# Kernel tuning notes

Hardware: AMD Instinct MI355X
Metric: run time of the kernel (lower is better)

The kernel has to match this reference:

```python
import jax, jax.numpy as jnp
import numpy as np

N_NODES = 50000
N_EDGES = 1000000
D_FEAT = 512
F_ATTN = 64
SLOPE = 0.2


def setup_inputs() -> dict:
    key = jax.random.key(0)
    ks = jax.random.split(key, 8)
    d_sim = jax.random.normal(ks[0], (N_NODES, D_FEAT), dtype=jnp.float32)
    m_sim = jax.random.normal(ks[1], (N_NODES, D_FEAT), dtype=jnp.float32)
    Wd = jax.random.normal(ks[2], (F_ATTN, D_FEAT), dtype=jnp.float32) * (1.0 / np.sqrt(D_FEAT))
    Wm = jax.random.normal(ks[3], (F_ATTN, D_FEAT), dtype=jnp.float32) * (1.0 / np.sqrt(D_FEAT))
    Wa = jax.random.normal(ks[4], (2 * F_ATTN,), dtype=jnp.float32) * (1.0 / np.sqrt(2 * F_ATTN))
    node_type = jax.random.randint(ks[5], (N_NODES,), 0, 2, dtype=jnp.int32)
    edge_src = jax.random.randint(ks[6], (N_EDGES,), 0, N_NODES, dtype=jnp.int32)
    edge_dst = jax.random.randint(ks[7], (N_EDGES,), 0, N_NODES, dtype=jnp.int32)
    return {"d_sim": d_sim, "m_sim": m_sim, "Wd": Wd, "Wm": Wm, "Wa": Wa,
            "node_type": node_type, "edge_src": edge_src, "edge_dst": edge_dst}


def reference(d_sim, m_sim, Wd, Wm, Wa, node_type, edge_src, edge_dst):
    # Per-node projection, type-dependent (type==1 -> disease fc, type==0 -> miRNA fc).
    # Dropout is 0.0 (identity).
    z_d = d_sim @ Wd.T                      # [N, F]
    z_m = m_sim @ Wm.T                      # [N, F]
    z = jnp.where(node_type[:, None] == 1, z_d, z_m)  # [N, F]

    # Edge attention: a = attn_fc(concat(z_src, z_dst)); split Wa to avoid materializing concat.
    zs = z[edge_src]                        # [E, F]
    e = zs @ Wa[:F_ATTN] + z[edge_dst] @ Wa[F_ATTN:]  # [E]
    e = jax.nn.leaky_relu(e, negative_slope=SLOPE)

    # Segment softmax over incoming edges of each dst node (DGL mailbox softmax).
    emax = jax.ops.segment_max(e, edge_dst, num_segments=N_NODES)  # [N]
    ex = jnp.exp(e - emax[edge_dst])                                # [E]
    denom = jax.ops.segment_sum(ex, edge_dst, num_segments=N_NODES)  # [N]
    alpha = ex / denom[edge_dst]                                    # [E]

    # Weighted neighbor aggregation + elu.
    h = jax.ops.segment_sum(alpha[:, None] * zs, edge_dst, num_segments=N_NODES)  # [N, F]
    return jax.nn.elu(h)
```

## Files before the change

kernel.cpp:

```cpp
#include <hip/hip_runtime.h>
#include <hip/hip_bf16.h>

#define N_NODES 50000
#define N_EDGES 1000000
#define D_FEAT 512
#define F_ATTN 64
#define SLOPE 0.2f
#define CAP 64
#define BINS 391
#define BINCAP 4096
#define BINBLK 123
#define EPB 8192

typedef __attribute__((ext_vector_type(8))) short short8;
typedef __attribute__((ext_vector_type(4))) float floatx4;

static __device__ __forceinline__ short f2bf(float x) {
    unsigned u = __float_as_uint(x);
    unsigned r = (u + 0x7FFFu + ((u >> 16) & 1u)) >> 16;
    return (short)r;
}

static __device__ __forceinline__ short8 cvt2(float4 x, float4 y) {
    short8 r;
    r[0] = f2bf(x.x); r[1] = f2bf(x.y); r[2] = f2bf(x.z); r[3] = f2bf(x.w);
    r[4] = f2bf(y.x); r[5] = f2bf(y.y); r[6] = f2bf(y.z); r[7] = f2bf(y.w);
    return r;
}

static __device__ __forceinline__ float bfu2f(unsigned short v) {
    return __uint_as_float((unsigned)v << 16);
}

static __device__ __forceinline__ void g2lds16(const void* g, void* l) {
    __builtin_amdgcn_global_load_lds(
        (const __attribute__((address_space(1))) void*)g,
        (__attribute__((address_space(3))) void*)l, 16, 0, 0);
}

__global__ __launch_bounds__(256) void wcvt_kernel(
    const float* __restrict__ Wd, const float* __restrict__ Wm,
    short* __restrict__ Wb, int* __restrict__ gcount)
{
    int i = blockIdx.x * 256 + threadIdx.x;
    int half = F_ATTN * D_FEAT;
    float v = (i < half) ? Wd[i] : Wm[i - half];
    Wb[i] = f2bf(v);
    if (i < BINS) gcount[i] = 0;
}

__global__ __launch_bounds__(1024) void bin_kernel(
    const int* __restrict__ edge_src, const int* __restrict__ edge_dst,
    int* __restrict__ gcount, int* __restrict__ bins)
{
    __shared__ int hist[BINS];
    __shared__ int base[BINS];
    int tid = threadIdx.x;
    if (tid < BINS) hist[tid] = 0;
    __syncthreads();

    int e0 = blockIdx.x * EPB + tid * 8;
    int myV[8], myB[8], myR[8];
    if (e0 + 8 <= N_EDGES) {
        int4 d0 = *(const int4*)(edge_dst + e0);
        int4 d1 = *(const int4*)(edge_dst + e0 + 4);
        int4 s0 = *(const int4*)(edge_src + e0);
        int4 s1v = *(const int4*)(edge_src + e0 + 4);
        int dd[8] = {d0.x, d0.y, d0.z, d0.w, d1.x, d1.y, d1.z, d1.w};
        int ss[8] = {s0.x, s0.y, s0.z, s0.w, s1v.x, s1v.y, s1v.z, s1v.w};
        #pragma unroll
        for (int k = 0; k < 8; k++) {
            myV[k] = (ss[k] << 7) | (dd[k] & 127);
            myB[k] = dd[k] >> 7;
            myR[k] = atomicAdd(&hist[myB[k]], 1);
        }
    } else {
        #pragma unroll
        for (int k = 0; k < 8; k++) {
            int e = e0 + k;
            if (e < N_EDGES) {
                int d = edge_dst[e];
                int s = edge_src[e];
                myV[k] = (s << 7) | (d & 127);
                myB[k] = d >> 7;
                myR[k] = atomicAdd(&hist[myB[k]], 1);
            } else { myV[k] = -1; myB[k] = 0; myR[k] = 0; }
        }
    }
    __syncthreads();
    if (tid < BINS) {
        int c = hist[tid];
        base[tid] = c ? atomicAdd(&gcount[tid], c) : 0;
    }
    __syncthreads();
    #pragma unroll
    for (int k = 0; k < 8; k++) {
        if (myV[k] >= 0) {
            int pos = base[myB[k]] + myR[k];
            if (pos < BINCAP) bins[(myB[k] << 12) + pos] = myV[k];
        }
    }
}

__global__ __launch_bounds__(256) void proj_kernel(
    const float* __restrict__ d_sim,
    const float* __restrict__ m_sim,
    const short* __restrict__ Wb,
    const float* __restrict__ Wa,
    const int* __restrict__ node_type,
    __hip_bfloat16* __restrict__ z,
    float* __restrict__ s1, float* __restrict__ s2)
{
    __shared__ char smem[65536];

    const int w      = threadIdx.x >> 6;
    const int lane   = threadIdx.x & 63;
    const int laneLo = lane & 15;
    const int quad   = lane >> 4;
    const int nodeBase = blockIdx.x * 64;

    const float* aP[4];
    #pragma unroll
    for (int i = 0; i < 4; i++) {
        int r = w * 16 + i * 4 + (lane >> 4);
        int arow = nodeBase + r; if (arow >= N_NODES) arow = N_NODES - 1;
        int lc = (lane & 15) ^ (r & 7);
        const float* src = (node_type[arow] == 1) ? d_sim : m_sim;
        aP[i] = src + (size_t)arow * D_FEAT + (lc << 2);
    }
    const short* bP[4];
    #pragma unroll
    for (int i = 0; i < 4; i++) {
        int r = (w * 4 + i) * 8 + (lane >> 3);
        int lc = (lane & 7) ^ (r & 7);
        bP[i] = Wb + (size_t)r * D_FEAT + (lc << 3);
    }

    floatx4 accD[4], accM[4];
    #pragma unroll
    for (int nt = 0; nt < 4; nt++) {
        accD[nt] = (floatx4){0.f, 0.f, 0.f, 0.f};
        accM[nt] = (floatx4){0.f, 0.f, 0.f, 0.f};
    }

    {
        char* b0 = smem;
        #pragma unroll
        for (int i = 0; i < 4; i++)
            g2lds16(aP[i], b0 + (w * 16 + i * 4) * 256);
        #pragma unroll
        for (int i = 0; i < 4; i++)
            g2lds16(bP[i], b0 + 16384 + (w * 4 + i) * 1024);
    }
    __syncthreads();

    const int rA  = w * 16 + laneLo;
    const int rx  = laneLo & 7;

    for (int t = 0; t < 8; t++) {
        if (t < 7) {
            char* nb = smem + ((t + 1) & 1) * 32768;
            int k0 = (t + 1) * 64;
            #pragma unroll
            for (int i = 0; i < 4; i++)
                g2lds16(aP[i] + k0, nb + (w * 16 + i * 4) * 256);
            #pragma unroll
            for (int i = 0; i < 4; i++)
                g2lds16(bP[i] + k0, nb + 16384 + (w * 4 + i) * 1024);
        }
        const char* cb = smem + (t & 1) * 32768;
        #pragma unroll
        for (int ks = 0; ks < 2; ks++) {
            int c0 = ks * 8 + quad * 2;
            float4 a0 = *(const float4*)(cb + rA * 256 + ((c0 ^ rx) << 4));
            float4 a1 = *(const float4*)(cb + rA * 256 + (((c0 + 1) ^ rx) << 4));
            short8 a = cvt2(a0, a1);
            int ch = ks * 4 + quad;
            int sl = (ch ^ rx) << 4;
            #pragma unroll
            for (int nt = 0; nt < 4; nt++) {
                const char* rowD = cb + 16384 + (nt * 16 + laneLo) * 128;
                short8 bD = *(const short8*)(rowD + sl);
                short8 bM = *(const short8*)(rowD + 64 * 128 + sl);
                accD[nt] = __builtin_amdgcn_mfma_f32_16x16x32_bf16(a, bD, accD[nt], 0, 0, 0);
                accM[nt] = __builtin_amdgcn_mfma_f32_16x16x32_bf16(a, bM, accM[nt], 0, 0, 0);
            }
        }
        __syncthreads();
    }

    float wa1[4], wa2[4];
    #pragma unroll
    for (int nt = 0; nt < 4; nt++) {
        wa1[nt] = Wa[nt * 16 + laneLo];
        wa2[nt] = Wa[F_ATTN + nt * 16 + laneLo];
    }

    #pragma unroll
    for (int reg = 0; reg < 4; reg++) {
        int node = nodeBase + w * 16 + quad * 4 + reg;
        bool ok = node < N_NODES;
        int isD = ok ? (node_type[node] == 1) : 0;
        float p1 = 0.f, p2 = 0.f;
        #pragma unroll
        for (int nt = 0; nt < 4; nt++) {
            float v = isD ? accD[nt][reg] : accM[nt][reg];
            if (ok) z[(size_t)node * F_ATTN + nt * 16 + laneLo] = __float2bfloat16(v);
            p1 += v * wa1[nt];
            p2 += v * wa2[nt];
        }
        #pragma unroll
        for (int off = 8; off; off >>= 1) {
            p1 += __shfl_xor(p1, off);
            p2 += __shfl_xor(p2, off);
        }
        if (ok && laneLo == 0) { s1[node] = p1; s2[node] = p2; }
    }
}

__global__ __launch_bounds__(1024) void agg_kernel(
    const int* __restrict__ gcount, const int* __restrict__ bins,
    const float* __restrict__ s1, const float* __restrict__ s2,
    const __hip_bfloat16* __restrict__ z, float* __restrict__ out)
{
    __shared__ unsigned short list[128 * CAP];
    __shared__ int lcnt[128];
    __shared__ float sW[16 * 64];
    __shared__ int   sS[16 * 64];
    int tid = threadIdx.x;
    int b   = blockIdx.x;
    if (tid < 128) lcnt[tid] = 0;
    __syncthreads();

    int bc = gcount[b]; if (bc > BINCAP) bc = BINCAP;
    for (int i = tid; i < bc; i += 1024) {
        int v = bins[(b << 12) + i];
        int n = v & 127;
        int s = v >> 7;
        int r = atomicAdd(&lcnt[n], 1);
        if (r < CAP) list[(n << 6) + r] = (unsigned short)s;
    }
    __syncthreads();

    int wv    = tid >> 6;
    int lane  = tid & 63;
    int fgrp  = (lane & 15) * 4;
    int ep    = lane >> 4;
    int wbase = wv * 64;

    for (int j8 = 0; j8 < 8; j8++) {
        int ln   = wv * 8 + j8;
        int node = (b << 7) + ln;
        bool nvalid = node < N_NODES;
        int cnt = nvalid ? lcnt[ln] : 0;
        if (cnt > CAP) cnt = CAP;

        int   src = 0;
        float wgt = 0.f;
        if (lane < cnt) {
            src = list[(ln << 6) + lane];
            float t = s1[src] + s2[node];
            float ev = (t > 0.f) ? t : SLOPE * t;
            wgt = __expf(ev);
        }
        float l = wgt;
        sW[wbase + lane] = wgt;
        sS[wbase + lane] = src;

        float4 h = {0.f, 0.f, 0.f, 0.f};
        for (int j = 0; j < cnt; j += 16) {
            #pragma unroll
            for (int u = 0; u < 16; u += 4) {
                int slot = wbase + j + u + ep;
                float wj = sW[slot];
                int   sj = sS[slot];
                ushort4 zz = *(const ushort4*)((const unsigned short*)z +
                                               (size_t)sj * F_ATTN + fgrp);
                h.x += wj * bfu2f(zz.x);
                h.y += wj * bfu2f(zz.y);
                h.z += wj * bfu2f(zz.z);
                h.w += wj * bfu2f(zz.w);
            }
        }
        #pragma unroll
        for (int off = 16; off <= 32; off <<= 1) {
            h.x += __shfl_xor(h.x, off);
            h.y += __shfl_xor(h.y, off);
            h.z += __shfl_xor(h.z, off);
            h.w += __shfl_xor(h.w, off);
        }
        #pragma unroll
        for (int off = 32; off; off >>= 1) l += __shfl_xor(l, off);

        if (ep == 0 && nvalid) {
            float inv = (cnt > 0) ? 1.f / l : 0.f;
            float4 o;
            float v;
            v = h.x * inv; o.x = (v > 0.f) ? v : (__expf(v) - 1.f);
            v = h.y * inv; o.y = (v > 0.f) ? v : (__expf(v) - 1.f);
            v = h.z * inv; o.z = (v > 0.f) ? v : (__expf(v) - 1.f);
            v = h.w * inv; o.w = (v > 0.f) ? v : (__expf(v) - 1.f);
            *(float4*)(out + (size_t)node * F_ATTN + fgrp) = o;
        }
    }
}

extern "C" void kernel_launch(void* const* d_in, const int* in_sizes, int n_in,
                              void* d_out, int out_size, void* d_ws, size_t ws_size,
                              hipStream_t stream) {
    const float* d_sim = (const float*)d_in[0];
    const float* m_sim = (const float*)d_in[1];
    const float* Wd    = (const float*)d_in[2];
    const float* Wm    = (const float*)d_in[3];
    const float* Wa    = (const float*)d_in[4];
    const int* node_type = (const int*)d_in[5];
    const int* edge_src  = (const int*)d_in[6];
    const int* edge_dst  = (const int*)d_in[7];
    float* out = (float*)d_out;

    char* ws = (char*)d_ws;
    __hip_bfloat16* z  = (__hip_bfloat16*)(ws + 0);
    float* s1          = (float*)(ws + 6400000);
    float* s2          = (float*)(ws + 6600000);
    int*   gcount      = (int*)  (ws + 6800000);
    short* Wb          = (short*)(ws + 7000000);
    int*   bins        = (int*)  (ws + 8388608);

    wcvt_kernel<<<(2 * F_ATTN * D_FEAT) / 256, 256, 0, stream>>>(Wd, Wm, Wb, gcount);
    bin_kernel<<<BINBLK, 1024, 0, stream>>>(edge_src, edge_dst, gcount, bins);
    proj_kernel<<<(N_NODES + 63) / 64, 256, 0, stream>>>(
        d_sim, m_sim, Wb, Wa, node_type, z, s1, s2);
    agg_kernel<<<BINS, 1024, 0, stream>>>(gcount, bins, s1, s2, z, out);
}
```

Baseline: 259.8 us.

## Load A operand directly to registers, fuse weight convert into bin kernel, trim agg loop

The projection kernel now reads the fp32 similarity rows straight into registers, double-buffered, instead of staging them through LDS. LDS use per block is halved and launch bounds ask for 4 blocks per CU to raise occupancy. The weight bf16 conversion moves into extra blocks of the binning kernel, and the counter reset becomes a memset, removing one kernel launch. The aggregation loop now steps in groups of 4 edges instead of 16 to skip padded work; the direct row loads may coalesce worse than the LDS path.

```diff
diff --git a/kernel.cpp b/kernel.cpp
--- a/kernel.cpp
+++ b/kernel.cpp
@@ -10,6 +10,7 @@
 #define BINS 391
 #define BINCAP 4096
 #define BINBLK 123
+#define WCVTBLK 64
 #define EPB 8192
 
 typedef __attribute__((ext_vector_type(8))) short short8;
@@ -38,28 +39,29 @@
         (__attribute__((address_space(3))) void*)l, 16, 0, 0);
 }
 
-__global__ __launch_bounds__(256) void wcvt_kernel(
-    const float* __restrict__ Wd, const float* __restrict__ Wm,
-    short* __restrict__ Wb, int* __restrict__ gcount)
-{
-    int i = blockIdx.x * 256 + threadIdx.x;
-    int half = F_ATTN * D_FEAT;
-    float v = (i < half) ? Wd[i] : Wm[i - half];
-    Wb[i] = f2bf(v);
-    if (i < BINS) gcount[i] = 0;
-}
-
 __global__ __launch_bounds__(1024) void bin_kernel(
     const int* __restrict__ edge_src, const int* __restrict__ edge_dst,
+    const float* __restrict__ Wd, const float* __restrict__ Wm,
+    short* __restrict__ Wb,
     int* __restrict__ gcount, int* __restrict__ bins)
 {
     __shared__ int hist[BINS];
     __shared__ int base[BINS];
     int tid = threadIdx.x;
+    int bid = blockIdx.x;
+
+    if (bid >= BINBLK) {
+        int i = (bid - BINBLK) * 1024 + tid;
+        int half = F_ATTN * D_FEAT;
+        float v = (i < half) ? Wd[i] : Wm[i - half];
+        Wb[i] = f2bf(v);
+        return;
+    }
+
     if (tid < BINS) hist[tid] = 0;
     __syncthreads();
 
-    int e0 = blockIdx.x * EPB + tid * 8;
+    int e0 = bid * EPB + tid * 8;
     int myV[8], myB[8], myR[8];
     if (e0 + 8 <= N_EDGES) {
         int4 d0 = *(const int4*)(edge_dst + e0);
@@ -102,7 +104,7 @@
     }
 }
 
-__global__ __launch_bounds__(256) void proj_kernel(
+__global__ __launch_bounds__(256, 4) void proj_kernel(
     const float* __restrict__ d_sim,
     const float* __restrict__ m_sim,
     const short* __restrict__ Wb,
@@ -111,7 +113,7 @@
     __hip_bfloat16* __restrict__ z,
     float* __restrict__ s1, float* __restrict__ s2)
 {
-    __shared__ char smem[65536];
+    __shared__ char smem[32768];
 
     const int w      = threadIdx.x >> 6;
     const int lane   = threadIdx.x & 63;
@@ -119,15 +121,10 @@
     const int quad   = lane >> 4;
     const int nodeBase = blockIdx.x * 64;
 
-    const float* aP[4];
-    #pragma unroll
-    for (int i = 0; i < 4; i++) {
-        int r = w * 16 + i * 4 + (lane >> 4);
-        int arow = nodeBase + r; if (arow >= N_NODES) arow = N_NODES - 1;
-        int lc = (lane & 15) ^ (r & 7);
-        const float* src = (node_type[arow] == 1) ? d_sim : m_sim;
-        aP[i] = src + (size_t)arow * D_FEAT + (lc << 2);
-    }
+    int arow = nodeBase + w * 16 + laneLo; if (arow >= N_NODES) arow = N_NODES - 1;
+    const float* rowPtr =
+        ((node_type[arow] == 1) ? d_sim : m_sim) + (size_t)arow * D_FEAT + quad * 8;
+
     const short* bP[4];
     #pragma unroll
     for (int i = 0; i < 4; i++) {
@@ -143,43 +140,41 @@
         accM[nt] = (floatx4){0.f, 0.f, 0.f, 0.f};
     }
 
+    float4 aR[2][4];
+    #pragma unroll
+    for (int c = 0; c < 4; c++)
+        aR[0][c] = *(const float4*)(rowPtr + ((c >> 1) * 32) + ((c & 1) * 4));
     {
         char* b0 = smem;
         #pragma unroll
         for (int i = 0; i < 4; i++)
-            g2lds16(aP[i], b0 + (w * 16 + i * 4) * 256);
-        #pragma unroll
-        for (int i = 0; i < 4; i++)
-            g2lds16(bP[i], b0 + 16384 + (w * 4 + i) * 1024);
-    }
-    __syncthreads();
-
-    const int rA  = w * 16 + laneLo;
-    const int rx  = laneLo & 7;
-
+            g2lds16(bP[i], b0 + (w * 4 + i) * 1024);
+    }
+    __syncthreads();
+
+    const int rx = laneLo & 7;
+
+    #pragma unroll
     for (int t = 0; t < 8; t++) {
         if (t < 7) {
-            char* nb = smem + ((t + 1) & 1) * 32768;
+            char* nb = smem + ((t + 1) & 1) * 16384;
             int k0 = (t + 1) * 64;
             #pragma unroll
             for (int i = 0; i < 4; i++)
-                g2lds16(aP[i] + k0, nb + (w * 16 + i * 4) * 256);
+                g2lds16(bP[i] + k0, nb + (w * 4 + i) * 1024);
             #pragma unroll
-            for (int i = 0; i < 4; i++)
-                g2lds16(bP[i] + k0, nb + 16384 + (w * 4 + i) * 1024);
-        }
-        const char* cb = smem + (t & 1) * 32768;
+            for (int c = 0; c < 4; c++)
+                aR[(t + 1) & 1][c] =
+                    *(const float4*)(rowPtr + k0 + ((c >> 1) * 32) + ((c & 1) * 4));
+        }
+        const char* cb = smem + (t & 1) * 16384;
         #pragma unroll
         for (int ks = 0; ks < 2; ks++) {
-            int c0 = ks * 8 + quad * 2;
-            float4 a0 = *(const float4*)(cb + rA * 256 + ((c0 ^ rx) << 4));
-            float4 a1 = *(const float4*)(cb + rA * 256 + (((c0 + 1) ^ rx) << 4));
-            short8 a = cvt2(a0, a1);
-            int ch = ks * 4 + quad;
-            int sl = (ch ^ rx) << 4;
+            short8 a = cvt2(aR[t & 1][ks * 2], aR[t & 1][ks * 2 + 1]);
+            int sl = ((ks * 4 + quad) ^ rx) << 4;
             #pragma unroll
             for (int nt = 0; nt < 4; nt++) {
-                const char* rowD = cb + 16384 + (nt * 16 + laneLo) * 128;
+                const char* rowD = cb + (nt * 16 + laneLo) * 128;
                 short8 bD = *(const short8*)(rowD + sl);
                 short8 bM = *(const short8*)(rowD + 64 * 128 + sl);
                 accD[nt] = __builtin_amdgcn_mfma_f32_16x16x32_bf16(a, bD, accD[nt], 0, 0, 0);
@@ -268,19 +263,17 @@
         sS[wbase + lane] = src;
 
         float4 h = {0.f, 0.f, 0.f, 0.f};
-        for (int j = 0; j < cnt; j += 16) {
-            #pragma unroll
-            for (int u = 0; u < 16; u += 4) {
-                int slot = wbase + j + u + ep;
-                float wj = sW[slot];
-                int   sj = sS[slot];
-                ushort4 zz = *(const ushort4*)((const unsigned short*)z +
-                                               (size_t)sj * F_ATTN + fgrp);
-                h.x += wj * bfu2f(zz.x);
-                h.y += wj * bfu2f(zz.y);
-                h.z += wj * bfu2f(zz.z);
-                h.w += wj * bfu2f(zz.w);
-            }
+        int usteps = (cnt + 3) >> 2;
+        for (int uu = 0; uu < usteps; uu++) {
+            int slot = wbase + (uu << 2) + ep;
+            float wj = sW[slot];
+            int   sj = sS[slot];
+            ushort4 zz = *(const ushort4*)((const unsigned short*)z +
+                                           (size_t)sj * F_ATTN + fgrp);
+            h.x += wj * bfu2f(zz.x);
+            h.y += wj * bfu2f(zz.y);
+            h.z += wj * bfu2f(zz.z);
+            h.w += wj * bfu2f(zz.w);
         }
         #pragma unroll
         for (int off = 16; off <= 32; off <<= 1) {
@@ -326,8 +319,9 @@
     short* Wb          = (short*)(ws + 7000000);
     int*   bins        = (int*)  (ws + 8388608);
 
-    wcvt_kernel<<<(2 * F_ATTN * D_FEAT) / 256, 256, 0, stream>>>(Wd, Wm, Wb, gcount);
-    bin_kernel<<<BINBLK, 1024, 0, stream>>>(edge_src, edge_dst, gcount, bins);
+    hipMemsetAsync(gcount, 0, BINS * sizeof(int), stream);
+    bin_kernel<<<BINBLK + WCVTBLK, 1024, 0, stream>>>(
+        edge_src, edge_dst, Wd, Wm, Wb, gcount, bins);
     proj_kernel<<<(N_NODES + 63) / 64, 256, 0, stream>>>(
         d_sim, m_sim, Wb, Wa, node_type, z, s1, s2);
     agg_kernel<<<BINS, 1024, 0, stream>>>(gcount, bins, s1, s2, z, out);
```

Result: slower. 266.2 us (+2.4%).
